# Performance work log

Measured on AMD Instinct MI355X. Metric: run time of the kernel, lower is better.

Reference implementation:

```python
import jax, jax.numpy as jnp
import numpy as np

B, N, D, H, DH = 2, 4096, 256, 8, 64   # batch, nodes, dim, heads, dim_head
INNER = H * DH
POLY_K = 3  # polynomial order -> coeffs [H, POLY_K+1]
LN_EPS = 1e-5


def setup_inputs() -> dict:
    key = jax.random.key(0)
    ks = jax.random.split(key, 8)
    s = 0.02
    return {
        "x": jax.random.normal(ks[0], (B, N, D), dtype=jnp.float32),
        "Wq": jax.random.normal(ks[1], (D, INNER), dtype=jnp.float32) * s,
        "Wk": jax.random.normal(ks[2], (D, INNER), dtype=jnp.float32) * s,
        "Wv": jax.random.normal(ks[3], (D, INNER), dtype=jnp.float32) * s,
        "Wo": jax.random.normal(ks[4], (INNER, D), dtype=jnp.float32) * s,
        "gamma": jnp.ones((DH,), dtype=jnp.float32),
        "beta": jnp.zeros((DH,), dtype=jnp.float32),
        "coeffs": jax.random.normal(ks[5], (H, POLY_K + 1), dtype=jnp.float32) * 0.5,
    }


def reference(x, Wq, Wk, Wv, Wo, gamma, beta, coeffs):
    b, n, d = x.shape
    h, dh = coeffs.shape[0], gamma.shape[0]
    # --- graph estimator: per-head softmax adjacency A = softmax(QK^T/sqrt(dh)) ---
    q = (x @ Wq).reshape(b, n, h, dh).transpose(0, 2, 1, 3)  # bhnd
    k = (x @ Wk).reshape(b, n, h, dh).transpose(0, 2, 1, 3)  # bhnd
    scale = jax.lax.rsqrt(jnp.asarray(dh, x.dtype))
    A = jax.nn.softmax(jnp.einsum('bhnd,bhmd->bhnm', q, k) * scale, axis=-1)
    # --- value projection + per-head LayerNorm over dim_head ---
    v = (x @ Wv).reshape(b, n, h, dh)
    mu = v.mean(axis=-1, keepdims=True)
    var = ((v - mu) ** 2).mean(axis=-1, keepdims=True)
    v = (v - mu) * jax.lax.rsqrt(var + LN_EPS) * gamma + beta
    v = v.transpose(0, 2, 1, 3)  # bhnd
    # --- polynomial graph filter: y = sum_k c[h,k] * A^k v ---
    y = coeffs[None, :, 0, None, None] * v
    t = v
    for kk in range(1, coeffs.shape[1]):
        t = jnp.einsum('bhnm,bhmd->bhnd', A, t)
        y = y + coeffs[None, :, kk, None, None] * t
    # --- merge heads + output projection ---
    merged = y.transpose(0, 2, 1, 3).reshape(b, n, h * dh)
    return merged @ Wo
```

## Files before the change

kernel.cpp:

```cpp
#include <hip/hip_runtime.h>
#include <stdint.h>

#define B_ 2
#define N_ 4096
#define D_ 256
#define H_ 8
#define DH_ 64
#define INNER_ 512
#define NBH 16
#define PAD 72
#define FPAD 80

typedef unsigned short ushort_t;
typedef __attribute__((ext_vector_type(8))) short short8;
typedef __attribute__((ext_vector_type(4))) float float4v;
typedef __attribute__((ext_vector_type(4))) unsigned short ushort4v;
typedef __attribute__((ext_vector_type(4))) unsigned int uint4v;

__device__ __forceinline__ ushort_t f2bf(float f) {
    union { float f; unsigned int u; } v; v.f = f;
    unsigned int r = v.u + 0x7FFFu + ((v.u >> 16) & 1u);
    return (ushort_t)(r >> 16);
}
__device__ __forceinline__ float bf2f(ushort_t u) {
    union { unsigned int u; float f; } v; v.u = ((unsigned int)u) << 16;
    return v.f;
}
__device__ __forceinline__ unsigned char f2fp8s(float f) {
    union { float f; unsigned int u; } v; v.f = f;
    unsigned int s = (v.u >> 24) & 0x80u;
    v.u &= 0x7FFFFFFFu;
    float a = v.f;
    if (a >= 448.f) return (unsigned char)(s | 0x7E);
    if (a < 0.015625f) {
        int m = (int)(a * 512.f + 0.5f);
        return (unsigned char)(s | (unsigned)m);
    }
    unsigned int u = v.u + 0x7FFFFu + ((v.u >> 20) & 1u);
    return (unsigned char)(s | (((u >> 20) & 0x7FF) - 960));
}
__device__ __forceinline__ float fexp2(float x) {
    float r;
    asm volatile("v_exp_f32 %0, %1\n\ts_nop 0" : "=v"(r) : "v"(x));
    return r;
}

__global__ __launch_bounds__(256) void prep_kernel(
    const float* __restrict__ x, const float* __restrict__ Wq,
    const float* __restrict__ Wk, const float* __restrict__ Wv,
    const float* __restrict__ Wo,
    ushort_t* __restrict__ xb, ushort_t* __restrict__ WqkvT,
    ushort_t* __restrict__ WoT) {
    int idx = blockIdx.x * 256 + threadIdx.x;
    const int total_x = B_ * N_ * D_;
    const int total_wqkv = 3 * INNER_ * D_;
    const int total_wo = D_ * INNER_;
    if (idx < total_x) { xb[idx] = f2bf(x[idx]); return; }
    idx -= total_x;
    if (idx < total_wqkv) {
        int n = idx >> 8, k = idx & 255;
        int which = n >> 9, nn = n & 511;
        const float* W = (which == 0) ? Wq : ((which == 1) ? Wk : Wv);
        WqkvT[idx] = f2bf(W[k * INNER_ + nn]);
        return;
    }
    idx -= total_wqkv;
    if (idx < total_wo) {
        int c = idx >> 9, k = idx & 511;
        WoT[idx] = f2bf(Wo[k * D_ + c]);
    }
}

__global__ __launch_bounds__(256) void proj_gemm(
    const ushort_t* __restrict__ xb, const ushort_t* __restrict__ WqkvT,
    const float* __restrict__ gamma, const float* __restrict__ beta,
    const float* __restrict__ coeffs,
    ushort_t* __restrict__ Qb, ushort_t* __restrict__ Kb,
    unsigned char* __restrict__ t0T, float* __restrict__ y) {
    __shared__ ushort_t As[128][PAD];
    __shared__ ushort_t Bs[128][PAD];
    int bid = blockIdx.x;
    int tileN = bid % 12, tileM = bid / 12;
    int tid = threadIdx.x;
    int w = tid >> 6, lane = tid & 63, q = lane >> 4, r = lane & 15;
    int wr = (w & 1) * 64, wc = (w >> 1) * 64;
    float4v acc[4][4];
    for (int i = 0; i < 4; i++)
        for (int j = 0; j < 4; j++)
            for (int e = 0; e < 4; e++) acc[i][j][e] = 0.f;

    for (int k0 = 0; k0 < 256; k0 += 64) {
        for (int it = 0; it < 4; it++) {
            int idx = tid + it * 256;
            int row = idx >> 3, kc = (idx & 7) * 8;
            *(short8*)&As[row][kc] =
                *(const short8*)&xb[(size_t)(tileM * 128 + row) * 256 + k0 + kc];
            *(short8*)&Bs[row][kc] =
                *(const short8*)&WqkvT[(size_t)(tileN * 128 + row) * 256 + k0 + kc];
        }
        __syncthreads();
        for (int kk = 0; kk < 64; kk += 32) {
            short8 a[4], b[4];
            for (int mi = 0; mi < 4; mi++)
                a[mi] = *(const short8*)&As[wr + mi * 16 + r][kk + q * 8];
            for (int ni = 0; ni < 4; ni++)
                b[ni] = *(const short8*)&Bs[wc + ni * 16 + r][kk + q * 8];
            for (int mi = 0; mi < 4; mi++)
                for (int ni = 0; ni < 4; ni++)
                    acc[mi][ni] = __builtin_amdgcn_mfma_f32_16x16x32_bf16(
                        a[mi], b[ni], acc[mi][ni], 0, 0, 0);
        }
        __syncthreads();
    }
    if (tileN < 8) {
        for (int mi = 0; mi < 4; mi++)
            for (int ni = 0; ni < 4; ni++)
                for (int reg = 0; reg < 4; reg++) {
                    int grow = tileM * 128 + wr + mi * 16 + q * 4 + reg;
                    int gcol = tileN * 128 + wc + ni * 16 + r;
                    float v = acc[mi][ni][reg];
                    int which = gcol >> 9, inner = gcol & 511;
                    int h = inner >> 6, d = inner & 63;
                    int b = grow >> 12, n = grow & 4095;
                    size_t off = (((size_t)(b * H_ + h)) * N_ + n) * DH_ + d;
                    if (which == 0) Qb[off] = f2bf(v * 0.18033688011112042f);
                    else Kb[off] = f2bf(v);
                }
    } else {
        int h = (((tileN - 8) * 128) + wc) >> 6;
        float c0 = coeffs[h * 4];
        float gm[4], bt[4];
#pragma unroll
        for (int ni = 0; ni < 4; ni++) {
            gm[ni] = gamma[ni * 16 + r];
            bt[ni] = beta[ni * 16 + r];
        }
#pragma unroll
        for (int mi = 0; mi < 4; mi++)
#pragma unroll
            for (int reg = 0; reg < 4; reg++) {
                float s = acc[mi][0][reg] + acc[mi][1][reg]
                        + acc[mi][2][reg] + acc[mi][3][reg];
                float s2 = acc[mi][0][reg] * acc[mi][0][reg]
                         + acc[mi][1][reg] * acc[mi][1][reg]
                         + acc[mi][2][reg] * acc[mi][2][reg]
                         + acc[mi][3][reg] * acc[mi][3][reg];
#pragma unroll
                for (int m = 1; m <= 8; m <<= 1) {
                    s  += __shfl_xor(s, m, 64);
                    s2 += __shfl_xor(s2, m, 64);
                }
                float mu = s * (1.f / 64.f);
                float var = s2 * (1.f / 64.f) - mu * mu;
                float rinv = rsqrtf(var + 1e-5f);
                int grow = tileM * 128 + wr + mi * 16 + q * 4 + reg;
                int b = grow >> 12, n = grow & 4095;
                int bh = b * H_ + h;
                float* yp = y + ((size_t)bh * N_ + n) * 64;
                unsigned char* tp = t0T + (size_t)bh * 64 * N_ + n;
#pragma unroll
                for (int ni = 0; ni < 4; ni++) {
                    float vln = (acc[mi][ni][reg] - mu) * rinv * gm[ni] + bt[ni];
                    yp[ni * 16 + r] = c0 * vln;
                    tp[(size_t)(ni * 16 + r) * 4096] = f2fp8s(vln);
                }
            }
    }
}


#define MFB(a, b, c) __builtin_amdgcn_mfma_f32_16x16x32_bf16(a, b, c, 0, 0, 0)
#define MFP(a, b, c) __builtin_amdgcn_mfma_f32_16x16x32_fp8_fp8(a, b, c, 0, 0, 0)

__device__ __forceinline__ long pk8(float4v x, float4v y) {
    int d0 = __builtin_amdgcn_cvt_pk_fp8_f32(fexp2(x[0]), fexp2(x[1]), 0, false);
    d0 = __builtin_amdgcn_cvt_pk_fp8_f32(fexp2(x[2]), fexp2(x[3]), d0, true);
    int d1 = __builtin_amdgcn_cvt_pk_fp8_f32(fexp2(y[0]), fexp2(y[1]), 0, false);
    d1 = __builtin_amdgcn_cvt_pk_fp8_f32(fexp2(y[2]), fexp2(y[3]), d1, true);
    return (long)(((unsigned long)(unsigned int)d1 << 32) | (unsigned int)d0);
}

#define WGBAR()                                                \
    do {                                                       \
        asm volatile("s_waitcnt lgkmcnt(0)" ::: "memory");     \
        __builtin_amdgcn_sched_barrier(0);                     \
        __builtin_amdgcn_s_barrier();                          \
        __builtin_amdgcn_sched_barrier(0);                     \
    } while (0)

#define COMPUTE32(KsX, TsX)                                                     \
    {                                                                           \
        short8 a0, a1;                                                          \
        float4v s00, s10, s20, s30, s01, s11, s21, s31;                         \
        a0 = *(const short8*)&KsX[r][q * 8];                                    \
        a1 = *(const short8*)&KsX[r][32 + q * 8];                               \
        s00 = MFB(a1, qf1, MFB(a0, qf0, zf));                                   \
        s01 = MFB(a1, qf3, MFB(a0, qf2, zf));                                   \
        a0 = *(const short8*)&KsX[16 + r][q * 8];                               \
        a1 = *(const short8*)&KsX[16 + r][32 + q * 8];                          \
        s10 = MFB(a1, qf1, MFB(a0, qf0, zf));                                   \
        s11 = MFB(a1, qf3, MFB(a0, qf2, zf));                                   \
        a0 = *(const short8*)&KsX[32 + r][q * 8];                               \
        a1 = *(const short8*)&KsX[32 + r][32 + q * 8];                          \
        s20 = MFB(a1, qf1, MFB(a0, qf0, zf));                                   \
        s21 = MFB(a1, qf3, MFB(a0, qf2, zf));                                   \
        a0 = *(const short8*)&KsX[48 + r][q * 8];                               \
        a1 = *(const short8*)&KsX[48 + r][32 + q * 8];                          \
        s30 = MFB(a1, qf1, MFB(a0, qf0, zf));                                   \
        s31 = MFB(a1, qf3, MFB(a0, qf2, zf));                                   \
        long eA0 = pk8(s00, s10), eB0 = pk8(s20, s30);                          \
        long eA1 = pk8(s01, s11), eB1 = pk8(s21, s31);                          \
        long b0 = *(const long*)&TsX[r][q * 8];                                 \
        long b1 = *(const long*)&TsX[16 + r][q * 8];                            \
        long b2 = *(const long*)&TsX[32 + r][q * 8];                            \
        long b3 = *(const long*)&TsX[48 + r][q * 8];                            \
        acc0[0] = MFP(eA0, b0, acc0[0]); acc1[0] = MFP(eA1, b0, acc1[0]);       \
        acc0[1] = MFP(eA0, b1, acc0[1]); acc1[1] = MFP(eA1, b1, acc1[1]);       \
        acc0[2] = MFP(eA0, b2, acc0[2]); acc1[2] = MFP(eA1, b2, acc1[2]);       \
        acc0[3] = MFP(eA0, b3, acc0[3]); acc1[3] = MFP(eA1, b3, acc1[3]);       \
        accs0 = MFP(eA0, bones, accs0);  accs1 = MFP(eA1, bones, accs1);        \
        b0 = *(const long*)&TsX[r][32 + q * 8];                                 \
        b1 = *(const long*)&TsX[16 + r][32 + q * 8];                            \
        b2 = *(const long*)&TsX[32 + r][32 + q * 8];                            \
        b3 = *(const long*)&TsX[48 + r][32 + q * 8];                            \
        acc0[0] = MFP(eB0, b0, acc0[0]); acc1[0] = MFP(eB1, b0, acc1[0]);       \
        acc0[1] = MFP(eB0, b1, acc0[1]); acc1[1] = MFP(eB1, b1, acc1[1]);       \
        acc0[2] = MFP(eB0, b2, acc0[2]); acc1[2] = MFP(eB1, b2, acc1[2]);       \
        acc0[3] = MFP(eB0, b3, acc0[3]); acc1[3] = MFP(eB1, b3, acc1[3]);       \
        accs0 = MFP(eB0, bones, accs0);  accs1 = MFP(eB1, bones, accs1);        \
    }

__global__ __launch_bounds__(512, 4) void poly_pass(
    const ushort_t* __restrict__ Qb, const ushort_t* __restrict__ Kb,
    const unsigned char* __restrict__ tinT, float* __restrict__ y,
    unsigned char* __restrict__ toutT, const float* __restrict__ coeffs,
    int kidx, int write_t) {
    __shared__ char smem[57344];
    typedef ushort_t KsArr[64][PAD];
    typedef unsigned char TsArr[64][FPAD];
    KsArr* Ks0 = (KsArr*)smem;
    KsArr* Ks1 = (KsArr*)(smem + 18432);
    TsArr* Ts0 = (TsArr*)(smem + 36864);
    TsArr* Ts1 = (TsArr*)(smem + 47104);

    int bid0 = blockIdx.x;
    int bid = ((bid0 & 7) << 6) | (bid0 >> 3);
    int bh = bid >> 5, ti = bid & 31;
    const ushort_t* Q = Qb + (size_t)bh * N_ * 64;
    const ushort_t* K = Kb + (size_t)bh * N_ * 64;
    const unsigned char* tin = tinT + (size_t)bh * 64 * N_;
    int tid = threadIdx.x, w = tid >> 6, lane = tid & 63, q = lane >> 4, r = lane & 15;
    int half = w >> 2, wsub = w & 3;
    const float4v zf = {0.f, 0.f, 0.f, 0.f};

    const ushort_t* qp = Q + (size_t)(ti * 128 + wsub * 32 + r) * 64 + q * 8;
    short8 qf0 = *(const short8*)qp;
    short8 qf1 = *(const short8*)(qp + 32);
    short8 qf2 = *(const short8*)(qp + 16 * 64);
    short8 qf3 = *(const short8*)(qp + 16 * 64 + 32);

    float4v acc0[4], acc1[4], accs0, accs1;
    for (int e = 0; e < 4; e++) { accs0[e] = 0.f; accs1[e] = 0.f; }
    for (int j = 0; j < 4; j++)
        for (int e = 0; e < 4; e++) { acc0[j][e] = 0.f; acc1[j][e] = 0.f; }
    const long bones = 0x3838383838383838L;

    int tl = tid & 255;
    int krow = tl >> 2, kpart = (tl & 3) * 16;
    int Lrow = (krow & 32) + ((krow & 4) << 2) + (krow & 3) + ((krow >> 3) & 3) * 4;
    const ushort_t* kp = K + (size_t)(half * 2048 + krow) * 64 + kpart;
    int srow = tl >> 2, scol = (tl & 3) * 16;
    const unsigned char* tp = tin + (size_t)srow * 4096 + half * 2048 + scol;

    {
        uint4v ka = *(const uint4v*)kp;
        uint4v kb = *(const uint4v*)(kp + 8);
        uint4v tv = *(const uint4v*)tp;
        *(uint4v*)&Ks0[half][Lrow][kpart] = ka;
        *(uint4v*)&Ks0[half][Lrow][kpart + 8] = kb;
        *(uint4v*)&Ts0[half][srow][scol] = tv;
    }
    uint4v pka = *(const uint4v*)(kp + 4096);
    uint4v pkb = *(const uint4v*)(kp + 4096 + 8);
    uint4v pt  = *(const uint4v*)(tp + 64);
    const ushort_t* kpl = kp + 2 * 4096;
    const unsigned char* tpl = tp + 2 * 64;
    WGBAR();

    for (int it = 0; it < 32; it += 2) {
        *(uint4v*)&Ks1[half][Lrow][kpart] = pka;
        *(uint4v*)&Ks1[half][Lrow][kpart + 8] = pkb;
        *(uint4v*)&Ts1[half][srow][scol] = pt;
        pka = *(const uint4v*)kpl;
        pkb = *(const uint4v*)(kpl + 8);
        pt  = *(const uint4v*)tpl;
        kpl += 4096; tpl += 64;
        COMPUTE32(Ks0[half], Ts0[half]);
        WGBAR();
        *(uint4v*)&Ks0[half][Lrow][kpart] = pka;
        *(uint4v*)&Ks0[half][Lrow][kpart + 8] = pkb;
        *(uint4v*)&Ts0[half][srow][scol] = pt;
        pka = *(const uint4v*)kpl;
        pkb = *(const uint4v*)(kpl + 8);
        pt  = *(const uint4v*)tpl;
        kpl += 4096; tpl += 64;
        COMPUTE32(Ks1[half], Ts1[half]);
        WGBAR();
    }

    float* ULDS = (float*)smem;
    unsigned char (*TT)[144] = (unsigned char(*)[144])(smem + 40960);

    if (half == 1) {
        float* ub = ULDS + (size_t)(wsub * 64 + lane) * 40;
#pragma unroll
        for (int j = 0; j < 4; j++) {
            *(float4v*)(ub + j * 4) = acc0[j];
            *(float4v*)(ub + 16 + j * 4) = acc1[j];
        }
        *(float4v*)(ub + 32) = accs0;
        *(float4v*)(ub + 36) = accs1;
    }
    WGBAR();
    if (half == 0) {
        const float* ub = ULDS + (size_t)(wsub * 64 + lane) * 40;
#pragma unroll
        for (int j = 0; j < 4; j++) {
            acc0[j] += *(const float4v*)(ub + j * 4);
            acc1[j] += *(const float4v*)(ub + 16 + j * 4);
        }
        accs0 += *(const float4v*)(ub + 32);
        accs1 += *(const float4v*)(ub + 36);

        int h = bh & 7;
        float ck = coeffs[h * 4 + kidx];
        float rinv0[4], rinv1[4];
#pragma unroll
        for (int reg = 0; reg < 4; reg++) {
            rinv0[reg] = 1.f / accs0[reg];
            rinv1[reg] = 1.f / accs1[reg];
        }
        float tv0[4][4], tv1[4][4];
#pragma unroll
        for (int ni = 0; ni < 4; ni++)
#pragma unroll
            for (int reg = 0; reg < 4; reg++) {
                tv0[ni][reg] = acc0[ni][reg] * rinv0[reg];
                tv1[ni][reg] = acc1[ni][reg] * rinv1[reg];
            }
#pragma unroll
        for (int reg = 0; reg < 4; reg++) {
            int il = wsub * 32 + q * 4 + reg;
            float* yp0 = y + ((size_t)bh * N_ + (size_t)ti * 128 + il) * 64;
            float* yp1 = yp0 + 16 * 64;
#pragma unroll
            for (int ni = 0; ni < 4; ni++) {
                yp0[ni * 16 + r] += ck * tv0[ni][reg];
                yp1[ni * 16 + r] += ck * tv1[ni][reg];
            }
        }
        if (write_t) {
#pragma unroll
            for (int ni = 0; ni < 4; ni++) {
                int p0 = __builtin_amdgcn_cvt_pk_fp8_f32(tv0[ni][0], tv0[ni][1], 0, false);
                p0 = __builtin_amdgcn_cvt_pk_fp8_f32(tv0[ni][2], tv0[ni][3], p0, true);
                *(unsigned int*)&TT[ni * 16 + r][wsub * 32 + q * 4] = (unsigned int)p0;
                int p1 = __builtin_amdgcn_cvt_pk_fp8_f32(tv1[ni][0], tv1[ni][1], 0, false);
                p1 = __builtin_amdgcn_cvt_pk_fp8_f32(tv1[ni][2], tv1[ni][3], p1, true);
                *(unsigned int*)&TT[ni * 16 + r][wsub * 32 + 16 + q * 4] = (unsigned int)p1;
            }
        }
    }
    if (write_t) {
        WGBAR();
        int drow = tid >> 3, dcol = (tid & 7) * 16;
        uint4v vv = *(const uint4v*)&TT[drow][dcol];
        *(uint4v*)&toutT[(size_t)bh * 64 * N_ + (size_t)drow * N_ + ti * 128 + dcol] = vv;
    }
}

__global__ __launch_bounds__(256) void out_gemm(
    const float* __restrict__ y, const ushort_t* __restrict__ WoT,
    float* __restrict__ out) {
    __shared__ ushort_t As[128][PAD];
    __shared__ ushort_t Bs[64][PAD];
    int bid = blockIdx.x;
    int tileN = bid & 3, tileM = bid >> 2;
    int tid = threadIdx.x, w = tid >> 6, lane = tid & 63, q = lane >> 4, r = lane & 15;
    int wr = w * 32;
    float4v acc[2][4];
    for (int i = 0; i < 2; i++)
        for (int j = 0; j < 4; j++)
            for (int e = 0; e < 4; e++) acc[i][j][e] = 0.f;

    for (int k0 = 0; k0 < 512; k0 += 64) {
        int h = k0 >> 6;
        for (int it = 0; it < 8; it++) {
            int idx = tid + it * 256;
            int row = idx >> 4, kc = (idx & 15) * 4;
            int grow = tileM * 128 + row;
            int b = grow >> 12, n = grow & 4095;
            const float4* src =
                (const float4*)&y[(((size_t)(b * H_ + h)) * N_ + n) * 64 + kc];
            float4 v = *src;
            ushort4v pv;
            pv[0] = f2bf(v.x); pv[1] = f2bf(v.y); pv[2] = f2bf(v.z); pv[3] = f2bf(v.w);
            *(ushort4v*)&As[row][kc] = pv;
        }
        for (int it = 0; it < 2; it++) {
            int idx = tid + it * 256;
            int row = idx >> 3, kc = (idx & 7) * 8;
            *(short8*)&Bs[row][kc] =
                *(const short8*)&WoT[(size_t)(tileN * 64 + row) * 512 + k0 + kc];
        }
        __syncthreads();
        for (int kk = 0; kk < 64; kk += 32) {
            short8 a[2], b[4];
            a[0] = *(const short8*)&As[wr + r][kk + q * 8];
            a[1] = *(const short8*)&As[wr + 16 + r][kk + q * 8];
            for (int ni = 0; ni < 4; ni++)
                b[ni] = *(const short8*)&Bs[ni * 16 + r][kk + q * 8];
            for (int mi = 0; mi < 2; mi++)
                for (int ni = 0; ni < 4; ni++)
                    acc[mi][ni] = __builtin_amdgcn_mfma_f32_16x16x32_bf16(
                        a[mi], b[ni], acc[mi][ni], 0, 0, 0);
        }
        __syncthreads();
    }
    for (int mi = 0; mi < 2; mi++)
        for (int reg = 0; reg < 4; reg++) {
            int grow = tileM * 128 + wr + mi * 16 + q * 4 + reg;
            for (int ni = 0; ni < 4; ni++) {
                int gcol = tileN * 64 + ni * 16 + r;
                out[(size_t)grow * 256 + gcol] = acc[mi][ni][reg];
            }
        }
}

extern "C" void kernel_launch(void* const* d_in, const int* in_sizes, int n_in,
                              void* d_out, int out_size, void* d_ws, size_t ws_size,
                              hipStream_t stream) {
    const float* x      = (const float*)d_in[0];
    const float* Wq     = (const float*)d_in[1];
    const float* Wk     = (const float*)d_in[2];
    const float* Wv     = (const float*)d_in[3];
    const float* Wo     = (const float*)d_in[4];
    const float* gamma  = (const float*)d_in[5];
    const float* beta   = (const float*)d_in[6];
    const float* coeffs = (const float*)d_in[7];
    float* out = (float*)d_out;

    char* ws = (char*)d_ws;
    size_t off = 0;
    auto alloc = [&](size_t bytes) -> void* {
        void* p = ws + off;
        off += (bytes + 255) & ~(size_t)255;
        return p;
    };
    ushort_t* xb    = (ushort_t*)alloc((size_t)B_ * N_ * D_ * 2);
    ushort_t* WqkvT = (ushort_t*)alloc((size_t)3 * INNER_ * D_ * 2);
    ushort_t* WoT   = (ushort_t*)alloc((size_t)D_ * INNER_ * 2);
    ushort_t* Qb    = (ushort_t*)alloc((size_t)NBH * N_ * DH_ * 2);
    ushort_t* Kb    = (ushort_t*)alloc((size_t)NBH * N_ * DH_ * 2);
    unsigned char* t0T = (unsigned char*)alloc((size_t)NBH * DH_ * N_);
    unsigned char* t1T = (unsigned char*)alloc((size_t)NBH * DH_ * N_);
    float*    y     = (float*)alloc((size_t)NBH * N_ * DH_ * 4);

    const int prep_total = B_ * N_ * D_ + 3 * INNER_ * D_ + D_ * INNER_;
    prep_kernel<<<(prep_total + 255) / 256, 256, 0, stream>>>(
        x, Wq, Wk, Wv, Wo, xb, WqkvT, WoT);
    proj_gemm<<<768, 256, 0, stream>>>(xb, WqkvT, gamma, beta, coeffs,
                                       Qb, Kb, t0T, y);

    poly_pass<<<NBH * 32, 512, 0, stream>>>(Qb, Kb, t0T, y, t1T, coeffs, 1, 1);
    poly_pass<<<NBH * 32, 512, 0, stream>>>(Qb, Kb, t1T, y, t0T, coeffs, 2, 1);
    poly_pass<<<NBH * 32, 512, 0, stream>>>(Qb, Kb, t0T, y, t1T, coeffs, 3, 0);

    out_gemm<<<256, 256, 0, stream>>>(y, WoT, out);
}
```

Measured before the change: 331.9 us.

## Load K fragments directly from global into registers, dropping K LDS staging

The poly pass no longer stages K tiles through shared memory. Each wave now reads its MFMA K fragments straight from global memory into registers, prefetched one phase ahead, and only the fp8 T tile stays double-buffered in LDS. This removes the K LDS writes and reads and shrinks shared memory, but every wave fetches K from global/L2 on its own with less coalescing, and register pressure goes up.

```diff
diff --git a/kernel.cpp b/kernel.cpp
--- a/kernel.cpp
+++ b/kernel.cpp
@@ -188,60 +188,62 @@
         __builtin_amdgcn_sched_barrier(0);                     \
     } while (0)
 
-#define COMPUTE32(KsX, TsX)                                                     \
-    {                                                                           \
-        short8 a0, a1;                                                          \
-        float4v s00, s10, s20, s30, s01, s11, s21, s31;                         \
-        a0 = *(const short8*)&KsX[r][q * 8];                                    \
-        a1 = *(const short8*)&KsX[r][32 + q * 8];                               \
-        s00 = MFB(a1, qf1, MFB(a0, qf0, zf));                                   \
-        s01 = MFB(a1, qf3, MFB(a0, qf2, zf));                                   \
-        a0 = *(const short8*)&KsX[16 + r][q * 8];                               \
-        a1 = *(const short8*)&KsX[16 + r][32 + q * 8];                          \
-        s10 = MFB(a1, qf1, MFB(a0, qf0, zf));                                   \
-        s11 = MFB(a1, qf3, MFB(a0, qf2, zf));                                   \
-        a0 = *(const short8*)&KsX[32 + r][q * 8];                               \
-        a1 = *(const short8*)&KsX[32 + r][32 + q * 8];                          \
-        s20 = MFB(a1, qf1, MFB(a0, qf0, zf));                                   \
-        s21 = MFB(a1, qf3, MFB(a0, qf2, zf));                                   \
-        a0 = *(const short8*)&KsX[48 + r][q * 8];                               \
-        a1 = *(const short8*)&KsX[48 + r][32 + q * 8];                          \
-        s30 = MFB(a1, qf1, MFB(a0, qf0, zf));                                   \
-        s31 = MFB(a1, qf3, MFB(a0, qf2, zf));                                   \
-        long eA0 = pk8(s00, s10), eB0 = pk8(s20, s30);                          \
-        long eA1 = pk8(s01, s11), eB1 = pk8(s21, s31);                          \
-        long b0 = *(const long*)&TsX[r][q * 8];                                 \
-        long b1 = *(const long*)&TsX[16 + r][q * 8];                            \
-        long b2 = *(const long*)&TsX[32 + r][q * 8];                            \
-        long b3 = *(const long*)&TsX[48 + r][q * 8];                            \
-        acc0[0] = MFP(eA0, b0, acc0[0]); acc1[0] = MFP(eA1, b0, acc1[0]);       \
-        acc0[1] = MFP(eA0, b1, acc0[1]); acc1[1] = MFP(eA1, b1, acc1[1]);       \
-        acc0[2] = MFP(eA0, b2, acc0[2]); acc1[2] = MFP(eA1, b2, acc1[2]);       \
-        acc0[3] = MFP(eA0, b3, acc0[3]); acc1[3] = MFP(eA1, b3, acc1[3]);       \
-        accs0 = MFP(eA0, bones, accs0);  accs1 = MFP(eA1, bones, accs1);        \
-        b0 = *(const long*)&TsX[r][32 + q * 8];                                 \
-        b1 = *(const long*)&TsX[16 + r][32 + q * 8];                            \
-        b2 = *(const long*)&TsX[32 + r][32 + q * 8];                            \
-        b3 = *(const long*)&TsX[48 + r][32 + q * 8];                            \
-        acc0[0] = MFP(eB0, b0, acc0[0]); acc1[0] = MFP(eB1, b0, acc1[0]);       \
-        acc0[1] = MFP(eB0, b1, acc0[1]); acc1[1] = MFP(eB1, b1, acc1[1]);       \
-        acc0[2] = MFP(eB0, b2, acc0[2]); acc1[2] = MFP(eB1, b2, acc1[2]);       \
-        acc0[3] = MFP(eB0, b3, acc0[3]); acc1[3] = MFP(eB1, b3, acc1[3]);       \
-        accs0 = MFP(eB0, bones, accs0);  accs1 = MFP(eB1, bones, accs1);        \
-    }
+#define POLY_PHASE(TsCur, TsNxt)                                               \
+    {                                                                          \
+        short8 c20 = *(const short8*)(kc + 2048);                              \
+        short8 c21 = *(const short8*)(kc + 2080);                              \
+        short8 c30 = *(const short8*)(kc + 2304);                              \
+        short8 c31 = *(const short8*)(kc + 2336);                              \
+        short8 nf00 = *(const short8*)(kc + 4096);                             \
+        short8 nf01 = *(const short8*)(kc + 4128);                             \
+        short8 nf10 = *(const short8*)(kc + 4352);                             \
+        short8 nf11 = *(const short8*)(kc + 4384);                             \
+        kc += 4096;                                                            \
+        *(uint4v*)&TsNxt[half][srow][scol] = pt;                               \
+        pt = *(const uint4v*)tpl;                                              \
+        tpl += 64;                                                             \
+        float4v s00, s01, s10, s11, s20, s21, s30, s31;                        \
+        s00 = MFB(pf01, qf1, MFB(pf00, qf0, zf));                              \
+        s01 = MFB(pf01, qf3, MFB(pf00, qf2, zf));                              \
+        s10 = MFB(pf11, qf1, MFB(pf10, qf0, zf));                              \
+        s11 = MFB(pf11, qf3, MFB(pf10, qf2, zf));                              \
+        s20 = MFB(c21, qf1, MFB(c20, qf0, zf));                                \
+        s21 = MFB(c21, qf3, MFB(c20, qf2, zf));                                \
+        s30 = MFB(c31, qf1, MFB(c30, qf0, zf));                                \
+        s31 = MFB(c31, qf3, MFB(c30, qf2, zf));                                \
+        long eA0 = pk8(s00, s10), eB0 = pk8(s20, s30);                         \
+        long eA1 = pk8(s01, s11), eB1 = pk8(s21, s31);                         \
+        long b0 = *(const long*)&TsCur[half][r][q * 8];                        \
+        long b1 = *(const long*)&TsCur[half][16 + r][q * 8];                   \
+        long b2 = *(const long*)&TsCur[half][32 + r][q * 8];                   \
+        long b3 = *(const long*)&TsCur[half][48 + r][q * 8];                   \
+        acc0[0] = MFP(eA0, b0, acc0[0]); acc1[0] = MFP(eA1, b0, acc1[0]);      \
+        acc0[1] = MFP(eA0, b1, acc0[1]); acc1[1] = MFP(eA1, b1, acc1[1]);      \
+        acc0[2] = MFP(eA0, b2, acc0[2]); acc1[2] = MFP(eA1, b2, acc1[2]);      \
+        acc0[3] = MFP(eA0, b3, acc0[3]); acc1[3] = MFP(eA1, b3, acc1[3]);      \
+        accs0 = MFP(eA0, bones, accs0);  accs1 = MFP(eA1, bones, accs1);       \
+        b0 = *(const long*)&TsCur[half][r][32 + q * 8];                        \
+        b1 = *(const long*)&TsCur[half][16 + r][32 + q * 8];                   \
+        b2 = *(const long*)&TsCur[half][32 + r][32 + q * 8];                   \
+        b3 = *(const long*)&TsCur[half][48 + r][32 + q * 8];                   \
+        acc0[0] = MFP(eB0, b0, acc0[0]); acc1[0] = MFP(eB1, b0, acc1[0]);      \
+        acc0[1] = MFP(eB0, b1, acc0[1]); acc1[1] = MFP(eB1, b1, acc1[1]);      \
+        acc0[2] = MFP(eB0, b2, acc0[2]); acc1[2] = MFP(eB1, b2, acc1[2]);      \
+        acc0[3] = MFP(eB0, b3, acc0[3]); acc1[3] = MFP(eB1, b3, acc1[3]);      \
+        accs0 = MFP(eB0, bones, accs0);  accs1 = MFP(eB1, bones, accs1);       \
+        pf00 = nf00; pf01 = nf01; pf10 = nf10; pf11 = nf11;                    \
+    }                                                                          \
+    WGBAR();
 
 __global__ __launch_bounds__(512, 4) void poly_pass(
     const ushort_t* __restrict__ Qb, const ushort_t* __restrict__ Kb,
     const unsigned char* __restrict__ tinT, float* __restrict__ y,
     unsigned char* __restrict__ toutT, const float* __restrict__ coeffs,
     int kidx, int write_t) {
-    __shared__ char smem[57344];
-    typedef ushort_t KsArr[64][PAD];
+    __shared__ char smem[50176];
     typedef unsigned char TsArr[64][FPAD];
-    KsArr* Ks0 = (KsArr*)smem;
-    KsArr* Ks1 = (KsArr*)(smem + 18432);
-    TsArr* Ts0 = (TsArr*)(smem + 36864);
-    TsArr* Ts1 = (TsArr*)(smem + 47104);
+    TsArr* Ts0 = (TsArr*)smem;
+    TsArr* Ts1 = (TsArr*)(smem + 10240);
 
     int bid0 = blockIdx.x;
     int bid = ((bid0 & 7) << 6) | (bid0 >> 3);
@@ -265,47 +267,28 @@
         for (int e = 0; e < 4; e++) { acc0[j][e] = 0.f; acc1[j][e] = 0.f; }
     const long bones = 0x3838383838383838L;
 
+    int Drow = ((r >> 2) & 3) * 8 + (r & 3);
+    const ushort_t* kc = K + (size_t)(half * 2048 + Drow) * 64 + q * 8;
+
     int tl = tid & 255;
-    int krow = tl >> 2, kpart = (tl & 3) * 16;
-    int Lrow = (krow & 32) + ((krow & 4) << 2) + (krow & 3) + ((krow >> 3) & 3) * 4;
-    const ushort_t* kp = K + (size_t)(half * 2048 + krow) * 64 + kpart;
     int srow = tl >> 2, scol = (tl & 3) * 16;
     const unsigned char* tp = tin + (size_t)srow * 4096 + half * 2048 + scol;
 
     {
-        uint4v ka = *(const uint4v*)kp;
-        uint4v kb = *(const uint4v*)(kp + 8);
         uint4v tv = *(const uint4v*)tp;
-        *(uint4v*)&Ks0[half][Lrow][kpart] = ka;
-        *(uint4v*)&Ks0[half][Lrow][kpart + 8] = kb;
         *(uint4v*)&Ts0[half][srow][scol] = tv;
     }
-    uint4v pka = *(const uint4v*)(kp + 4096);
-    uint4v pkb = *(const uint4v*)(kp + 4096 + 8);
-    uint4v pt  = *(const uint4v*)(tp + 64);
-    const ushort_t* kpl = kp + 2 * 4096;
+    uint4v pt = *(const uint4v*)(tp + 64);
     const unsigned char* tpl = tp + 2 * 64;
+    short8 pf00 = *(const short8*)(kc);
+    short8 pf01 = *(const short8*)(kc + 32);
+    short8 pf10 = *(const short8*)(kc + 256);
+    short8 pf11 = *(const short8*)(kc + 288);
     WGBAR();
 
     for (int it = 0; it < 32; it += 2) {
-        *(uint4v*)&Ks1[half][Lrow][kpart] = pka;
-        *(uint4v*)&Ks1[half][Lrow][kpart + 8] = pkb;
-        *(uint4v*)&Ts1[half][srow][scol] = pt;
-        pka = *(const uint4v*)kpl;
-        pkb = *(const uint4v*)(kpl + 8);
-        pt  = *(const uint4v*)tpl;
-        kpl += 4096; tpl += 64;
-        COMPUTE32(Ks0[half], Ts0[half]);
-        WGBAR();
-        *(uint4v*)&Ks0[half][Lrow][kpart] = pka;
-        *(uint4v*)&Ks0[half][Lrow][kpart + 8] = pkb;
-        *(uint4v*)&Ts0[half][srow][scol] = pt;
-        pka = *(const uint4v*)kpl;
-        pkb = *(const uint4v*)(kpl + 8);
-        pt  = *(const uint4v*)tpl;
-        kpl += 4096; tpl += 64;
-        COMPUTE32(Ks1[half], Ts1[half]);
-        WGBAR();
+        POLY_PHASE(Ts0, Ts1);
+        POLY_PHASE(Ts1, Ts0);
     }
 
     float* ULDS = (float*)smem;
```

New measurement: 511.0 us. 53.9% more time.
